# Kernel tuning notes

Measured on AMD Instinct MI355X. Metric: run time of the kernel, lower is better.

Reference implementation:

```python
import jax, jax.numpy as jnp
import numpy as np

# Config constants (match init_kwargs / config)
B = 16        # config.BATCH_SIZE
T = 2048      # config.TRAIN_LEN
C = 256       # input channels (input_shape[-1])
K = 8         # kernel_size
F = 256       # nb_filters
DIL = 4       # dilation_rate


def setup_inputs() -> dict:
    key = jax.random.key(0)
    k1, k2, k3 = jax.random.split(key, 3)
    inputs = jax.random.normal(k1, (B, T, C), dtype=jnp.float32)
    kernel = jax.random.normal(k2, (C, K, F), dtype=jnp.float32) * 0.05
    bias = jax.random.normal(k3, (F,), dtype=jnp.float32) * 0.05
    return {"inputs": inputs, "kernel": kernel, "bias": bias}


def reference(inputs, kernel, bias):
    # Original TF layer computes, per (b,t,k,f):
    #   raw[b,t,k,f] = sum_c (x[b,t,c] * kernel[c,k,f] + bias[f])
    #               = conv[b,t,k,f] + C * bias[f]
    # (bias is added BEFORE the reduce_sum over the channel axis, so it is
    #  scaled by C — we reproduce that quirk faithfully.)
    # Then each (t,k) slice is scatter-added to output time t + k*dilation
    # (the gather_nd + zero-pad construction in TF implements exactly this
    #  dilated transposed-conv scatter; non-matching positions gather zeros),
    # and finally the last T timesteps are kept.
    Bq, Tq, Cq = inputs.shape
    Kq, Fq = kernel.shape[1], kernel.shape[2]
    conv = jnp.einsum('btc,ckf->btkf', inputs, kernel) + jnp.asarray(Cq, inputs.dtype) * bias
    L = Tq + (Kq - 1) * DIL  # final_time_len
    # scatter positions: out[i + j*DIL] += conv[:, i, j, :]
    pos = (jnp.arange(Tq)[:, None] + DIL * jnp.arange(Kq)[None, :]).reshape(-1)  # (T*K,)
    out = jnp.zeros((Bq, L, Fq), dtype=conv.dtype)
    out = out.at[:, pos, :].add(conv.reshape(Bq, Tq * Kq, Fq))
    return out[:, -Tq:, :]
```

## Files before the change

kernel.cpp:

```cpp
#include <hip/hip_runtime.h>
#include <hip/hip_bf16.h>


#define B_    16
#define T_    2048
#define C_    256
#define KT    8
#define F_    256
#define SH    28
#define BT    256
#define FW    64
#define ROWS  (BT + SH)
#define CH    32
#define CHW   (ROWS * CH)
#define NTASK (ROWS * 4)

typedef __attribute__((ext_vector_type(8))) short short8;
typedef __attribute__((ext_vector_type(4))) float floatx4;

__global__ __launch_bounds__(256) void wprep_kernel(const float* __restrict__ W,
                                                    ushort* __restrict__ Wf) {
    const int tid  = threadIdx.x;
    const int fid  = blockIdx.x * 4 + (tid >> 6);
    const int lane = tid & 63;
    const int g    = fid & 15;
    const int S    = fid >> 4;
    const int j    = S & 7, cs = S >> 3;
    const int c0   = cs * 32 + (lane >> 4) * 8;
    const int f    = g * 16 + (lane & 15);
    short8 pk;
    #pragma unroll
    for (int i = 0; i < 8; ++i) {
        __hip_bfloat16 h = __float2bfloat16(W[((c0 + i) * KT + j) * F_ + f]);
        pk[i] = *reinterpret_cast<const short*>(&h);
    }
    *reinterpret_cast<short8*>(Wf + (size_t)fid * 512 + lane * 8) = pk;
}

__device__ inline short8 cvt8(float4 a, float4 b) {
    float v[8] = {a.x, a.y, a.z, a.w, b.x, b.y, b.z, b.w};
    short8 r;
    #pragma unroll
    for (int i = 0; i < 8; ++i) {
        __hip_bfloat16 h = __float2bfloat16(v[i]);
        r[i] = *reinterpret_cast<const short*>(&h);
    }
    return r;
}

__global__ __launch_bounds__(256, 2) void deconv_kernel(
        const float* __restrict__ x, const ushort* __restrict__ Wf,
        const float* __restrict__ bias, float* __restrict__ out) {
    __shared__ ushort xs[2 * CHW];
    const int bid  = blockIdx.x;
    const int ft   = bid >> 7;
    const int tb   = bid & 127;
    const int b    = tb >> 3;
    const int t0   = (tb & 7) * BT;
    const int tid  = threadIdx.x;
    const int lane = tid & 63, w = tid >> 6;
    const int l16  = lane & 15, q = lane >> 4;

    float4 SA[5], SB[5];

#define STAGE_LOAD(cs_) do {                                                   \
        _Pragma("unroll")                                                      \
        for (int k = 0; k < 5; ++k) {                                          \
            const int task = tid + k * 256;                                    \
            const int row_ = task >> 2, g_ = task & 3;                         \
            SA[k] = make_float4(0.f, 0.f, 0.f, 0.f);                           \
            SB[k] = make_float4(0.f, 0.f, 0.f, 0.f);                           \
            if (task < NTASK && t0 + row_ < T_) {                              \
                const float4* p_ = reinterpret_cast<const float4*>(            \
                    x + ((size_t)(b * T_ + t0 + row_) * C_ +                   \
                         (cs_) * CH + g_ * 8));                                \
                SA[k] = p_[0]; SB[k] = p_[1];                                  \
            } } } while (0)

#define STAGE_WRITE(buf_) do {                                                 \
        ushort* d_ = xs + (buf_) * CHW;                                        \
        _Pragma("unroll")                                                      \
        for (int k = 0; k < 5; ++k) {                                          \
            const int task = tid + k * 256;                                    \
            const int row_ = task >> 2, g_ = task & 3;                         \
            if (task < NTASK)                                                  \
                *reinterpret_cast<short8*>(                                    \
                    d_ + row_ * CH + ((g_ ^ (row_ & 3)) * 8)) =                \
                    cvt8(SA[k], SB[k]);                                        \
        } } while (0)

#define LOAD_A(buf_, j_, arr) do {                                             \
        const int rb_ = SH - 4 * (j_) + w * 64 + l16;                          \
        _Pragma("unroll")                                                      \
        for (int mf = 0; mf < 4; ++mf) {                                       \
            const int row_ = rb_ + mf * 16;                                    \
            arr[mf] = *reinterpret_cast<const short8*>(                        \
                xs + (buf_) * CHW + row_ * CH + ((q ^ (row_ & 3)) * 8));       \
        } } while (0)

#define LOAD_B(S_, arr) do {                                                   \
        const ushort* p_ = wbase + (size_t)(S_) * 8192;                        \
        _Pragma("unroll")                                                      \
        for (int nf = 0; nf < 4; ++nf)                                         \
            arr[nf] = *reinterpret_cast<const short8*>(p_ + nf * 512);         \
        } while (0)

#define DO_MFMA(aa, bb) do {                                                   \
        _Pragma("unroll")                                                      \
        for (int mf = 0; mf < 4; ++mf)                                         \
            _Pragma("unroll")                                                  \
            for (int nf = 0; nf < 4; ++nf)                                     \
                acc[mf][nf] = __builtin_amdgcn_mfma_f32_16x16x32_bf16(         \
                    aa[mf], bb[nf], acc[mf][nf], 0, 0, 0);                     \
        } while (0)

    const ushort* wbase = Wf + (size_t)(ft * 4) * 512 + lane * 8;

    float bf4[4];
    #pragma unroll
    for (int nf = 0; nf < 4; ++nf) bf4[nf] = bias[ft * 64 + nf * 16 + l16];

    floatx4 acc[4][4];
    #pragma unroll
    for (int mf = 0; mf < 4; ++mf)
        #pragma unroll
        for (int nf = 0; nf < 4; ++nf)
            acc[mf][nf] = (floatx4){0.f, 0.f, 0.f, 0.f};

    short8 aA[4], aB[4], bA[4], bB[4];

    STAGE_LOAD(0);
    LOAD_B(0, bA);
    LOAD_B(1, bB);
    STAGE_WRITE(0);
    __syncthreads();

    for (int cs = 0; cs < 8; ++cs) {
        const int buf = cs & 1;
        if (cs < 7) STAGE_LOAD(cs + 1);
        LOAD_A(buf, 0, aA);
        LOAD_A(buf, 1, aB);
        #pragma unroll
        for (int j = 0; j < 8; j += 2) {
            const int S = cs * 8 + j;
            __builtin_amdgcn_s_setprio(1);
            DO_MFMA(aA, bA);
            __builtin_amdgcn_s_setprio(0);
            if (j < 6) LOAD_A(buf, j + 2, aA);
            LOAD_B((S + 2) & 63, bA);
            __builtin_amdgcn_s_setprio(1);
            DO_MFMA(aB, bB);
            __builtin_amdgcn_s_setprio(0);
            if (j < 6) LOAD_A(buf, j + 3, aB);
            LOAD_B((S + 3) & 63, bB);
        }
        if (cs < 7) STAGE_WRITE(buf ^ 1);
        __syncthreads();
    }

    #pragma unroll
    for (int mf = 0; mf < 4; ++mf) {
        #pragma unroll
        for (int nf = 0; nf < 4; ++nf) {
            const int f = ft * 64 + nf * 16 + l16;
            #pragma unroll
            for (int r = 0; r < 4; ++r) {
                const int t = t0 + w * 64 + mf * 16 + q * 4 + r;
                const int jmin = (t < T_ - SH) ? 0 : (((t - (T_ - SH)) >> 2) + 1);
                out[(size_t)(b * T_ + t) * F_ + f] =
                    acc[mf][nf][r] + (float)(8 - jmin) * 256.0f * bf4[nf];
            }
        }
    }
#undef STAGE_LOAD
#undef STAGE_WRITE
#undef LOAD_A
#undef LOAD_B
#undef DO_MFMA
}

extern "C" void kernel_launch(void* const* d_in, const int* in_sizes, int n_in,
                              void* d_out, int out_size, void* d_ws, size_t ws_size,
                              hipStream_t stream) {
    const float* x    = (const float*)d_in[0];
    const float* W    = (const float*)d_in[1];
    const float* bias = (const float*)d_in[2];
    float* out = (float*)d_out;
    ushort* Wf = (ushort*)d_ws;

    wprep_kernel<<<256, 256, 0, stream>>>(W, Wf);
    deconv_kernel<<<512, 256, 0, stream>>>(x, Wf, bias, out);
}
```

Baseline: 44.83 us.

## Interleave staged x loads and LDS writes across MFMA steps, deepen B prefetch

Rebuilds the inner loop into a software pipeline. The global loads and bf16 LDS writes for the next channel chunk are now spread across the eight j-steps instead of being issued in bursts. The weight prefetch moves to a 4-deep ring, and the first A fragment of the next chunk is loaded right after the barrier. The LDS swizzle also changes to key on (row>>1)&3 to cut bank conflicts for the strided row access. The goal is to hide global and LDS latency behind the MFMAs, at the cost of more live registers, which may pressure occupancy under launch_bounds(256,2).

```diff
diff --git a/kernel.cpp b/kernel.cpp
--- a/kernel.cpp
+++ b/kernel.cpp
@@ -9,7 +9,6 @@
 #define F_    256
 #define SH    28
 #define BT    256
-#define FW    64
 #define ROWS  (BT + SH)
 #define CH    32
 #define CHW   (ROWS * CH)
@@ -63,30 +62,25 @@
 
     float4 SA[5], SB[5];
 
-#define STAGE_LOAD(cs_) do {                                                   \
-        _Pragma("unroll")                                                      \
-        for (int k = 0; k < 5; ++k) {                                          \
-            const int task = tid + k * 256;                                    \
-            const int row_ = task >> 2, g_ = task & 3;                         \
-            SA[k] = make_float4(0.f, 0.f, 0.f, 0.f);                           \
-            SB[k] = make_float4(0.f, 0.f, 0.f, 0.f);                           \
-            if (task < NTASK && t0 + row_ < T_) {                              \
-                const float4* p_ = reinterpret_cast<const float4*>(            \
-                    x + ((size_t)(b * T_ + t0 + row_) * C_ +                   \
-                         (cs_) * CH + g_ * 8));                                \
-                SA[k] = p_[0]; SB[k] = p_[1];                                  \
-            } } } while (0)
+#define STAGE_LOAD_K(cs_, k_) do {                                             \
+        const int task_ = tid + (k_) * 256;                                    \
+        const int row_  = task_ >> 2, g_ = task_ & 3;                          \
+        SA[k_] = make_float4(0.f, 0.f, 0.f, 0.f);                              \
+        SB[k_] = make_float4(0.f, 0.f, 0.f, 0.f);                              \
+        if (task_ < NTASK && t0 + row_ < T_) {                                 \
+            const float4* p_ = reinterpret_cast<const float4*>(                \
+                x + ((size_t)(b * T_ + t0 + row_) * C_ + (cs_) * CH + g_ * 8));\
+            SA[k_] = p_[0]; SB[k_] = p_[1];                                    \
+        } } while (0)
 
-#define STAGE_WRITE(buf_) do {                                                 \
-        ushort* d_ = xs + (buf_) * CHW;                                        \
-        _Pragma("unroll")                                                      \
-        for (int k = 0; k < 5; ++k) {                                          \
-            const int task = tid + k * 256;                                    \
-            const int row_ = task >> 2, g_ = task & 3;                         \
-            if (task < NTASK)                                                  \
-                *reinterpret_cast<short8*>(                                    \
-                    d_ + row_ * CH + ((g_ ^ (row_ & 3)) * 8)) =                \
-                    cvt8(SA[k], SB[k]);                                        \
+#define STAGE_WRITE_K(buf_, k_) do {                                           \
+        const int task_ = tid + (k_) * 256;                                    \
+        const int row_  = task_ >> 2, g_ = task_ & 3;                          \
+        if (task_ < NTASK) {                                                   \
+            const int sl_ = g_ ^ ((row_ >> 1) & 3);                            \
+            *reinterpret_cast<short8*>(                                        \
+                xs + (buf_) * CHW + row_ * CH + sl_ * 8) =                     \
+                cvt8(SA[k_], SB[k_]);                                          \
         } } while (0)
 
 #define LOAD_A(buf_, j_, arr) do {                                             \
@@ -94,8 +88,9 @@
         _Pragma("unroll")                                                      \
         for (int mf = 0; mf < 4; ++mf) {                                       \
             const int row_ = rb_ + mf * 16;                                    \
+            const int sl_  = q ^ ((row_ >> 1) & 3);                            \
             arr[mf] = *reinterpret_cast<const short8*>(                        \
-                xs + (buf_) * CHW + row_ * CH + ((q ^ (row_ & 3)) * 8));       \
+                xs + (buf_) * CHW + row_ * CH + sl_ * 8);                      \
         } } while (0)
 
 #define LOAD_B(S_, arr) do {                                                   \
@@ -127,35 +122,33 @@
         for (int nf = 0; nf < 4; ++nf)
             acc[mf][nf] = (floatx4){0.f, 0.f, 0.f, 0.f};
 
-    short8 aA[4], aB[4], bA[4], bB[4];
+    short8 aR[2][4];
+    short8 bR[4][4];
 
-    STAGE_LOAD(0);
-    LOAD_B(0, bA);
-    LOAD_B(1, bB);
-    STAGE_WRITE(0);
+    STAGE_LOAD_K(0, 0); STAGE_LOAD_K(0, 1); STAGE_LOAD_K(0, 2);
+    STAGE_LOAD_K(0, 3); STAGE_LOAD_K(0, 4);
+    LOAD_B(0, bR[0]);
+    LOAD_B(1, bR[1]);
+    STAGE_WRITE_K(0, 0); STAGE_WRITE_K(0, 1); STAGE_WRITE_K(0, 2);
+    STAGE_WRITE_K(0, 3); STAGE_WRITE_K(0, 4);
     __syncthreads();
+    LOAD_A(0, 0, aR[0]);
 
     for (int cs = 0; cs < 8; ++cs) {
         const int buf = cs & 1;
-        if (cs < 7) STAGE_LOAD(cs + 1);
-        LOAD_A(buf, 0, aA);
-        LOAD_A(buf, 1, aB);
+        const int Sb  = cs * 8;
         #pragma unroll
-        for (int j = 0; j < 8; j += 2) {
-            const int S = cs * 8 + j;
+        for (int j = 0; j < 8; ++j) {
+            LOAD_B((Sb + j + 2) & 63, bR[(j + 2) & 3]);
+            if (j < 7) LOAD_A(buf, j + 1, aR[(j + 1) & 1]);
+            if (j < 5 && cs < 7) STAGE_LOAD_K(cs + 1, j);
+            if (j >= 3 && cs < 7) STAGE_WRITE_K(buf ^ 1, j - 3);
             __builtin_amdgcn_s_setprio(1);
-            DO_MFMA(aA, bA);
+            DO_MFMA(aR[j & 1], bR[j & 3]);
             __builtin_amdgcn_s_setprio(0);
-            if (j < 6) LOAD_A(buf, j + 2, aA);
-            LOAD_B((S + 2) & 63, bA);
-            __builtin_amdgcn_s_setprio(1);
-            DO_MFMA(aB, bB);
-            __builtin_amdgcn_s_setprio(0);
-            if (j < 6) LOAD_A(buf, j + 3, aB);
-            LOAD_B((S + 3) & 63, bB);
         }
-        if (cs < 7) STAGE_WRITE(buf ^ 1);
         __syncthreads();
+        if (cs < 7) LOAD_A(buf ^ 1, 0, aR[0]);
     }
 
     #pragma unroll
@@ -172,8 +165,8 @@
             }
         }
     }
-#undef STAGE_LOAD
-#undef STAGE_WRITE
+#undef STAGE_LOAD_K
+#undef STAGE_WRITE_K
 #undef LOAD_A
 #undef LOAD_B
 #undef DO_MFMA
```

After: 44.43 us. No clear change (-0.9%).

## Use single-wave blocks over 64-row tiles and drop block barriers

Applied to the files above, without the earlier changes.

Each block shrinks from four waves covering 256 time rows to one wave covering 64 rows, and the grid grows to 2048 blocks. The tile order changes so neighbouring blocks share the batch and time tile across filter tiles. With one wave per block, the __syncthreads calls go away. The LDS swizzle now uses a row>>1 XOR pattern, and the A/B fragment loads are software-pipelined with a 4-deep B ring and a 2-deep A ring. The cost is that the 28-row halo is reloaded and converted per 64 rows instead of per 256, which raises input traffic and conversion work.

```diff
diff --git a/kernel.cpp b/kernel.cpp
--- a/kernel.cpp
+++ b/kernel.cpp
@@ -8,8 +8,7 @@
 #define KT    8
 #define F_    256
 #define SH    28
-#define BT    256
-#define FW    64
+#define BT    64
 #define ROWS  (BT + SH)
 #define CH    32
 #define CHW   (ROWS * CH)
@@ -48,29 +47,28 @@
     return r;
 }
 
-__global__ __launch_bounds__(256, 2) void deconv_kernel(
+__global__ __launch_bounds__(64, 2) void deconv_kernel(
         const float* __restrict__ x, const ushort* __restrict__ Wf,
         const float* __restrict__ bias, float* __restrict__ out) {
     __shared__ ushort xs[2 * CHW];
     const int bid  = blockIdx.x;
-    const int ft   = bid >> 7;
-    const int tb   = bid & 127;
-    const int b    = tb >> 3;
-    const int t0   = (tb & 7) * BT;
-    const int tid  = threadIdx.x;
-    const int lane = tid & 63, w = tid >> 6;
+    const int ft   = bid & 3;
+    const int tb   = bid >> 2;
+    const int b    = tb & 15;
+    const int t0   = (tb >> 4) * BT;
+    const int lane = threadIdx.x;
     const int l16  = lane & 15, q = lane >> 4;
 
-    float4 SA[5], SB[5];
+    float4 SA[6], SB[6];
 
 #define STAGE_LOAD(cs_) do {                                                   \
         _Pragma("unroll")                                                      \
-        for (int k = 0; k < 5; ++k) {                                          \
-            const int task = tid + k * 256;                                    \
-            const int row_ = task >> 2, g_ = task & 3;                         \
+        for (int k = 0; k < 6; ++k) {                                          \
+            const int task_ = lane + k * 64;                                   \
+            const int row_  = task_ >> 2, g_ = task_ & 3;                      \
             SA[k] = make_float4(0.f, 0.f, 0.f, 0.f);                           \
             SB[k] = make_float4(0.f, 0.f, 0.f, 0.f);                           \
-            if (task < NTASK && t0 + row_ < T_) {                              \
+            if (task_ < NTASK && t0 + row_ < T_) {                             \
                 const float4* p_ = reinterpret_cast<const float4*>(            \
                     x + ((size_t)(b * T_ + t0 + row_) * C_ +                   \
                          (cs_) * CH + g_ * 8));                                \
@@ -80,22 +78,23 @@
 #define STAGE_WRITE(buf_) do {                                                 \
         ushort* d_ = xs + (buf_) * CHW;                                        \
         _Pragma("unroll")                                                      \
-        for (int k = 0; k < 5; ++k) {                                          \
-            const int task = tid + k * 256;                                    \
-            const int row_ = task >> 2, g_ = task & 3;                         \
-            if (task < NTASK)                                                  \
+        for (int k = 0; k < 6; ++k) {                                          \
+            const int task_ = lane + k * 64;                                   \
+            const int row_  = task_ >> 2, g_ = task_ & 3;                      \
+            if (task_ < NTASK) {                                               \
+                const int sl_ = g_ ^ ((row_ >> 1) & 3);                        \
                 *reinterpret_cast<short8*>(                                    \
-                    d_ + row_ * CH + ((g_ ^ (row_ & 3)) * 8)) =                \
-                    cvt8(SA[k], SB[k]);                                        \
-        } } while (0)
+                    d_ + row_ * CH + sl_ * 8) = cvt8(SA[k], SB[k]);            \
+            } } } while (0)
 
 #define LOAD_A(buf_, j_, arr) do {                                             \
-        const int rb_ = SH - 4 * (j_) + w * 64 + l16;                          \
+        const int rb_ = SH - 4 * (j_) + l16;                                   \
         _Pragma("unroll")                                                      \
         for (int mf = 0; mf < 4; ++mf) {                                       \
             const int row_ = rb_ + mf * 16;                                    \
+            const int sl_  = q ^ ((row_ >> 1) & 3);                            \
             arr[mf] = *reinterpret_cast<const short8*>(                        \
-                xs + (buf_) * CHW + row_ * CH + ((q ^ (row_ & 3)) * 8));       \
+                xs + (buf_) * CHW + row_ * CH + sl_ * 8);                      \
         } } while (0)
 
 #define LOAD_B(S_, arr) do {                                                   \
@@ -127,35 +126,31 @@
         for (int nf = 0; nf < 4; ++nf)
             acc[mf][nf] = (floatx4){0.f, 0.f, 0.f, 0.f};
 
-    short8 aA[4], aB[4], bA[4], bB[4];
+    short8 aR[2][4];
+    short8 bR[4][4];
 
     STAGE_LOAD(0);
-    LOAD_B(0, bA);
-    LOAD_B(1, bB);
+    LOAD_B(0, bR[0]);
+    LOAD_B(1, bR[1]);
     STAGE_WRITE(0);
-    __syncthreads();
+    LOAD_A(0, 0, aR[0]);
 
     for (int cs = 0; cs < 8; ++cs) {
         const int buf = cs & 1;
+        const int Sb  = cs * 8;
         if (cs < 7) STAGE_LOAD(cs + 1);
-        LOAD_A(buf, 0, aA);
-        LOAD_A(buf, 1, aB);
         #pragma unroll
-        for (int j = 0; j < 8; j += 2) {
-            const int S = cs * 8 + j;
+        for (int j = 0; j < 8; ++j) {
+            LOAD_B((Sb + j + 2) & 63, bR[(j + 2) & 3]);
+            if (j < 7) LOAD_A(buf, j + 1, aR[(j + 1) & 1]);
             __builtin_amdgcn_s_setprio(1);
-            DO_MFMA(aA, bA);
+            DO_MFMA(aR[j & 1], bR[j & 3]);
             __builtin_amdgcn_s_setprio(0);
-            if (j < 6) LOAD_A(buf, j + 2, aA);
-            LOAD_B((S + 2) & 63, bA);
-            __builtin_amdgcn_s_setprio(1);
-            DO_MFMA(aB, bB);
-            __builtin_amdgcn_s_setprio(0);
-            if (j < 6) LOAD_A(buf, j + 3, aB);
-            LOAD_B((S + 3) & 63, bB);
         }
-        if (cs < 7) STAGE_WRITE(buf ^ 1);
-        __syncthreads();
+        if (cs < 7) {
+            STAGE_WRITE(buf ^ 1);
+            LOAD_A(buf ^ 1, 0, aR[0]);
+        }
     }
 
     #pragma unroll
@@ -165,7 +160,7 @@
             const int f = ft * 64 + nf * 16 + l16;
             #pragma unroll
             for (int r = 0; r < 4; ++r) {
-                const int t = t0 + w * 64 + mf * 16 + q * 4 + r;
+                const int t = t0 + mf * 16 + q * 4 + r;
                 const int jmin = (t < T_ - SH) ? 0 : (((t - (T_ - SH)) >> 2) + 1);
                 out[(size_t)(b * T_ + t) * F_ + f] =
                     acc[mf][nf][r] + (float)(8 - jmin) * 256.0f * bf4[nf];
@@ -189,5 +184,5 @@
     ushort* Wf = (ushort*)d_ws;
 
     wprep_kernel<<<256, 256, 0, stream>>>(W, Wf);
-    deconv_kernel<<<512, 256, 0, stream>>>(x, Wf, bias, out);
+    deconv_kernel<<<2048, 64, 0, stream>>>(x, Wf, bias, out);
 }
```

Result: slower. 50.02 us (+11.6%).
